# Kernel tuning notes

Measured on AMD Instinct MI355X. Metric: run time of the kernel, lower is better.

Reference implementation:

```python
import jax, jax.numpy as jnp
import numpy as np

EMBED_DIM = 1024
NUM_HEADS = 16
HEAD_DIM = EMBED_DIM // NUM_HEADS


def setup_inputs() -> dict:
    key = jax.random.key(0)
    ks = jax.random.split(key, 9)
    B, S, E = 4, 2048, EMBED_DIM
    # xavier_uniform bound for square [E, E] weights
    bound = float(np.sqrt(6.0 / (E + E)))
    def w(k):
        return jax.random.uniform(k, (E, E), jnp.float32, -bound, bound)
    return {
        "x": jax.random.normal(ks[0], (B, S, E), jnp.float32),
        "Wq": w(ks[1]), "bq": jnp.zeros((E,), jnp.float32),
        "Wk": w(ks[2]), "bk": jnp.zeros((E,), jnp.float32),
        "Wv": w(ks[3]), "bv": jnp.zeros((E,), jnp.float32),
        "Wo": w(ks[4]), "bo": jnp.zeros((E,), jnp.float32),
    }


def reference(x, Wq, bq, Wk, bk, Wv, bv, Wo, bo):
    B, S, E = x.shape
    H, D = NUM_HEADS, HEAD_DIM
    # Linear projections (torch Linear: x @ W.T + b)
    q = (x @ Wq.T + bq).reshape(B, S, H, D)
    k = (x @ Wk.T + bk).reshape(B, S, H, D)
    v = (x @ Wv.T + bv).reshape(B, S, H, D)
    # per-head scaled dot-product attention (vectorized over heads)
    scores = jnp.einsum("bqhd,bkhd->bhqk", q, k) / jnp.sqrt(jnp.float32(D))
    attn = jax.nn.softmax(scores, axis=-1)
    o = jnp.einsum("bhqk,bkhd->bqhd", attn, v).reshape(B, S, E)
    return o @ Wo.T + bo
```

## Files before the change

kernel.cpp:

```cpp
#include <hip/hip_runtime.h>
#include <stdint.h>

typedef unsigned short u16;
typedef short bf16x8 __attribute__((ext_vector_type(8)));
typedef float f32x4 __attribute__((ext_vector_type(4)));

#define B_ 4
#define S_ 2048
#define H_ 16
#define D_ 64
#define E_ 1024
#define M_ (B_ * S_)

static __device__ __forceinline__ u16 f2bf(float f) {
  uint32_t u = __builtin_bit_cast(uint32_t, f);
  u += 0x7fffu + ((u >> 16) & 1u);
  return (u16)(u >> 16);
}
static __device__ __forceinline__ u16 hu16(float f) {
  return (u16)((__builtin_bit_cast(uint32_t, f) + 0x8000u) >> 16);
}
static __device__ __forceinline__ uint32_t pack2bf(float a, float b) {
  return (uint32_t)f2bf(a) | ((uint32_t)f2bf(b) << 16);
}

static __device__ __forceinline__ void gld_lds16(const void* g, void* l) {
  __builtin_amdgcn_global_load_lds(
      (const __attribute__((address_space(1))) void*)(uintptr_t)g,
      (__attribute__((address_space(3))) void*)(uint32_t)(uintptr_t)l, 16, 0, 0);
}

template <int ctrl>
static __device__ __forceinline__ float dpp_mov(float x) {
  return __builtin_bit_cast(float,
      __builtin_amdgcn_update_dpp(0, __builtin_bit_cast(int, x), ctrl, 0xF, 0xF, true));
}
static __device__ __forceinline__ float rowsum16(float x) {
  x += dpp_mov<0xB1>(x);
  x += dpp_mov<0x4E>(x);
  x += dpp_mov<0x141>(x);
  x += dpp_mov<0x140>(x);
  return x;
}

#define NXE (M_ * E_)
#define NWE (E_ * E_)
__global__ __launch_bounds__(256) void cvt_all(const float* __restrict__ x,
                                               const float* __restrict__ Wq,
                                               const float* __restrict__ Wk,
                                               const float* __restrict__ Wv,
                                               const float* __restrict__ Wo,
                                               u16* __restrict__ ws) {
  int i = (blockIdx.x * 256 + threadIdx.x) * 8;
  const float* src;
  u16* dst = ws + i;
  if (i < NXE) { src = x + i; }
  else if (i < NXE + NWE)     { src = Wq + (i - NXE); }
  else if (i < NXE + 2 * NWE) { src = Wk + (i - NXE - NWE); }
  else if (i < NXE + 3 * NWE) { src = Wv + (i - NXE - 2 * NWE); }
  else                        { src = Wo + (i - NXE - 3 * NWE); }
  float4 a = *(const float4*)src;
  float4 b = *(const float4*)(src + 4);
  struct __align__(16) U8 { u16 h[8]; } u;
  u.h[0] = f2bf(a.x); u.h[1] = f2bf(a.y); u.h[2] = f2bf(a.z); u.h[3] = f2bf(a.w);
  u.h[4] = f2bf(b.x); u.h[5] = f2bf(b.y); u.h[6] = f2bf(b.z); u.h[7] = f2bf(b.w);
  *(U8*)dst = u;
}

template <int KIND, typename OutT>
static __device__ __forceinline__ void gemm128(const u16* __restrict__ A,
                                               const u16* __restrict__ W,
                                               const float* __restrict__ bias,
                                               OutT* __restrict__ C, int m0, int n0,
                                               float scale, u16* As, u16* Bs) {
  const int tid = threadIdx.x;
  const int wave = tid >> 6, lane = tid & 63;
  const int col16 = lane & 15, quad = lane >> 4;
  const int wm = wave >> 1, wn = wave & 1;

  f32x4 acc[4][4] = {};

  const int r0 = tid >> 3;
  const int sg8 = ((tid & 7) ^ (r0 & 7)) * 8;
  const u16* ga = A + (size_t)(m0 + r0) * E_ + sg8;
  const u16* gb = W + (size_t)(n0 + r0) * E_ + sg8;
  u16* lA = As + wave * 512;
  u16* lB = Bs + wave * 512;

  for (int k0 = 0; k0 < E_; k0 += 64) {
    __syncthreads();
#pragma unroll
    for (int i = 0; i < 4; i++) {
      gld_lds16(ga + (size_t)(i * 32) * E_ + k0, lA + i * 2048);
      gld_lds16(gb + (size_t)(i * 32) * E_ + k0, lB + i * 2048);
    }
    asm volatile("s_waitcnt vmcnt(0)" ::: "memory");
    __syncthreads();

    bf16x8 af[4][2], bw[4][2];
#pragma unroll
    for (int mt = 0; mt < 4; mt++)
#pragma unroll
      for (int ks = 0; ks < 2; ks++)
        af[mt][ks] = *(const bf16x8*)&As[(wm * 64 + mt * 16 + col16) * 64 +
                                         (((ks * 4 + quad) ^ (col16 & 7)) * 8)];
#pragma unroll
    for (int nt = 0; nt < 4; nt++)
#pragma unroll
      for (int ks = 0; ks < 2; ks++)
        bw[nt][ks] = *(const bf16x8*)&Bs[(wn * 64 + nt * 16 + col16) * 64 +
                                         (((ks * 4 + quad) ^ (col16 & 7)) * 8)];
#pragma unroll
    for (int ks = 0; ks < 2; ks++)
#pragma unroll
      for (int a = 0; a < 4; a++)
#pragma unroll
        for (int b = 0; b < 4; b++) {
          if constexpr (KIND == 2)
            acc[a][b] = __builtin_amdgcn_mfma_f32_16x16x32_bf16(af[a][ks], bw[b][ks], acc[a][b], 0, 0, 0);
          else
            acc[a][b] = __builtin_amdgcn_mfma_f32_16x16x32_bf16(bw[a][ks], af[b][ks], acc[a][b], 0, 0, 0);
        }
  }

  if constexpr (KIND == 2) {
#pragma unroll
    for (int a = 0; a < 4; a++) {
      int t = m0 + wm * 64 + a * 16 + quad * 4;
      int bb = t >> 11, s = t & (S_ - 1);
#pragma unroll
      for (int b = 0; b < 4; b++) {
        int oc = n0 + wn * 64 + b * 16 + col16;
        int h = oc >> 6, d = oc & 63;
        float bv = bias[oc];
        uint2 pk = {pack2bf(acc[a][b][0] + bv, acc[a][b][1] + bv),
                    pack2bf(acc[a][b][2] + bv, acc[a][b][3] + bv)};
        *(uint2*)&C[(((size_t)(bb * H_ + h) * D_ + d) * S_) + s] = pk;
      }
    }
  } else {
#pragma unroll
    for (int b = 0; b < 4; b++) {
      int row = m0 + wm * 64 + b * 16 + col16;
#pragma unroll
      for (int a = 0; a < 4; a++) {
        int nc = n0 + wn * 64 + a * 16 + quad * 4;
        float4 bv = *(const float4*)&bias[nc];
        float v0 = (acc[a][b][0] + bv.x) * scale;
        float v1 = (acc[a][b][1] + bv.y) * scale;
        float v2 = (acc[a][b][2] + bv.z) * scale;
        float v3 = (acc[a][b][3] + bv.w) * scale;
        if constexpr (KIND == 0) {
          uint2 pk = {pack2bf(v0, v1), pack2bf(v2, v3)};
          *(uint2*)&((u16*)C)[(size_t)row * E_ + nc] = pk;
        } else {
          float4 pk = {v0, v1, v2, v3};
          *(float4*)&((float*)C)[(size_t)row * E_ + nc] = pk;
        }
      }
    }
  }
}

__global__ __launch_bounds__(256) void gemm_qkv(const u16* __restrict__ xb,
                                                const u16* __restrict__ wq, const u16* __restrict__ wk,
                                                const u16* __restrict__ wv,
                                                const float* __restrict__ bq, const float* __restrict__ bk,
                                                const float* __restrict__ bv,
                                                u16* __restrict__ Qb, u16* __restrict__ Kb,
                                                u16* __restrict__ Vtb) {
  __shared__ __align__(16) u16 As[128 * 64];
  __shared__ __align__(16) u16 Bs[128 * 64];
  const int mat = blockIdx.x >> 3;
  const int n0 = (blockIdx.x & 7) * 128;
  const int m0 = blockIdx.y * 128;
  if (mat == 0)
    gemm128<0, u16>(xb, wq, bq, Qb, m0, n0, 0.125f * 1.44269504f, As, Bs);
  else if (mat == 1)
    gemm128<0, u16>(xb, wk, bk, Kb, m0, n0, 1.0f, As, Bs);
  else
    gemm128<2, u16>(xb, wv, bv, Vtb, m0, n0, 1.0f, As, Bs);
}

__global__ __launch_bounds__(256) void gemm_out(const u16* __restrict__ Ob,
                                                const u16* __restrict__ wob,
                                                const float* __restrict__ bo,
                                                float* __restrict__ out) {
  __shared__ __align__(16) u16 As[128 * 64];
  __shared__ __align__(16) u16 Bs[128 * 64];
  gemm128<1, float>(Ob, wob, bo, out, blockIdx.y * 128, blockIdx.x * 128, 1.0f, As, Bs);
}

__global__ __launch_bounds__(256) void flash_attn(const u16* __restrict__ Q,
                                                  const u16* __restrict__ K,
                                                  const u16* __restrict__ Vt,
                                                  u16* __restrict__ O) {
  __shared__ __align__(16) u16 Ks[2][64 * 64];
  __shared__ __align__(16) u16 Vs[64 * 64];
  __shared__ __align__(16) u16 Ps[4][32 * 72];
  const int bid = blockIdx.x;
  const int qt = bid >> 6, h = bid & 15, b = (bid >> 4) & 3;
  const int tid = threadIdx.x;
  const int wave = tid >> 6, lane = tid & 63;
  const int col16 = lane & 15, quad = lane >> 4;

  bf16x8 qf[2][2];
  const int qrow = qt * 128 + wave * 32;
#pragma unroll
  for (int mt = 0; mt < 2; mt++) {
    const u16* qp = Q + ((size_t)(b * S_ + qrow + mt * 16 + col16) * H_ + h) * D_ + quad * 8;
    qf[mt][0] = *(const bf16x8*)qp;
    qf[mt][1] = *(const bf16x8*)(qp + 32);
  }

  f32x4 o_acc[2][4] = {};
  float l_i[2][4] = {};

  const int srow = tid >> 3;
  const int sgrp = (tid & 7) ^ (srow & 7);
  const u16* Kbase = K + ((size_t)(b * S_) * H_ + h) * D_;
  const u16* Vbase = Vt + ((size_t)(b * H_ + h) * D_) * S_;
  u16* Pw = &Ps[wave][0];

  auto stageK = [&](int kb, int buf) {
#pragma unroll
    for (int i = 0; i < 2; i++)
      gld_lds16(Kbase + (size_t)(kb * 64 + i * 32 + srow) * (H_ * D_) + sgrp * 8,
                &Ks[buf][i * 2048 + wave * 512]);
  };
  auto stageV = [&](int kb) {
#pragma unroll
    for (int i = 0; i < 2; i++)
      gld_lds16(Vbase + (size_t)(i * 32 + srow) * S_ + kb * 64 + sgrp * 8,
                &Vs[i * 2048 + wave * 512]);
  };

  stageK(0, 0);
  for (int kb = 0; kb < S_ / 64; kb++) {
    const int cur = kb & 1;
    asm volatile("s_barrier" ::: "memory");
    stageV(kb);
    stageK((kb + 1) & 31, cur ^ 1);
    asm volatile("s_waitcnt vmcnt(4)" ::: "memory");
    asm volatile("s_barrier" ::: "memory");
    const u16* KsC = Ks[cur];

    f32x4 sacc[2][4] = {};
#pragma unroll
    for (int ks = 0; ks < 2; ks++) {
      bf16x8 kf[4];
#pragma unroll
      for (int nt = 0; nt < 4; nt++)
        kf[nt] = *(const bf16x8*)&KsC[(nt * 16 + col16) * 64 +
                                      (((ks * 4 + quad) ^ (col16 & 7)) * 8)];
#pragma unroll
      for (int mt = 0; mt < 2; mt++)
#pragma unroll
        for (int nt = 0; nt < 4; nt++)
          sacc[mt][nt] = __builtin_amdgcn_mfma_f32_16x16x32_bf16(qf[mt][ks], kf[nt], sacc[mt][nt], 0, 0, 0);
    }

#pragma unroll
    for (int mt = 0; mt < 2; mt++) {
#pragma unroll
      for (int e = 0; e < 4; e++) {
        float p0 = __builtin_amdgcn_exp2f(sacc[mt][0][e]);
        float p1 = __builtin_amdgcn_exp2f(sacc[mt][1][e]);
        float p2 = __builtin_amdgcn_exp2f(sacc[mt][2][e]);
        float p3 = __builtin_amdgcn_exp2f(sacc[mt][3][e]);
        l_i[mt][e] += (p0 + p1) + (p2 + p3);
        const int r = mt * 16 + quad * 4 + e;
        const int ro = r * 72;
        const int cb = col16 + ((r & 8) ? 16 : 0);
        Pw[ro + (cb & 63)] = hu16(p0);
        Pw[ro + ((cb + 16) & 63)] = hu16(p1);
        Pw[ro + ((cb + 32) & 63)] = hu16(p2);
        Pw[ro + ((cb + 48) & 63)] = hu16(p3);
      }
    }
    asm volatile("s_waitcnt lgkmcnt(0)" ::: "memory");
    asm volatile("s_waitcnt vmcnt(2)" ::: "memory");
    asm volatile("s_barrier" ::: "memory");

#pragma unroll
    for (int ks = 0; ks < 2; ks++) {
      bf16x8 pf[2], vf[4];
#pragma unroll
      for (int mt = 0; mt < 2; mt++)
        pf[mt] = *(const bf16x8*)&Pw[(mt * 16 + col16) * 72 +
                                     (((ks * 4 + quad + ((col16 >> 3) << 1)) & 7) * 8)];
#pragma unroll
      for (int nt = 0; nt < 4; nt++)
        vf[nt] = *(const bf16x8*)&Vs[(nt * 16 + col16) * 64 +
                                     (((ks * 4 + quad) ^ (col16 & 7)) * 8)];
#pragma unroll
      for (int mt = 0; mt < 2; mt++)
#pragma unroll
        for (int nt = 0; nt < 4; nt++)
          o_acc[mt][nt] = __builtin_amdgcn_mfma_f32_16x16x32_bf16(pf[mt], vf[nt], o_acc[mt][nt], 0, 0, 0);
    }
  }

#pragma unroll
  for (int mt = 0; mt < 2; mt++) {
#pragma unroll
    for (int e = 0; e < 4; e++) {
      float inv = 1.f / rowsum16(l_i[mt][e]);
      int s = qrow + mt * 16 + quad * 4 + e;
#pragma unroll
      for (int nt = 0; nt < 4; nt++)
        O[((size_t)(b * S_ + s) * H_ + h) * D_ + nt * 16 + col16] =
            f2bf(o_acc[mt][nt][e] * inv);
    }
  }
}

extern "C" void kernel_launch(void* const* d_in, const int* in_sizes, int n_in,
                              void* d_out, int out_size, void* d_ws, size_t ws_size,
                              hipStream_t stream) {
  (void)in_sizes; (void)n_in; (void)out_size; (void)ws_size;
  const float* x  = (const float*)d_in[0];
  const float* Wq = (const float*)d_in[1];
  const float* bq = (const float*)d_in[2];
  const float* Wk = (const float*)d_in[3];
  const float* bk = (const float*)d_in[4];
  const float* Wv = (const float*)d_in[5];
  const float* bv = (const float*)d_in[6];
  const float* Wo = (const float*)d_in[7];
  const float* bo = (const float*)d_in[8];
  float* out = (float*)d_out;

  const size_t NX = (size_t)M_ * E_;
  const size_t NW = (size_t)E_ * E_;
  u16* xb  = (u16*)d_ws;
  u16* wqb = xb + NX;
  u16* wkb = wqb + NW;
  u16* wvb = wkb + NW;
  u16* wob = wvb + NW;
  u16* Qb  = wob + NW;
  u16* Kb  = Qb + NX;
  u16* Vtb = Kb + NX;
  u16* Ob  = Vtb + NX;

  cvt_all<<<(NX + 4 * NW) / 2048, 256, 0, stream>>>(x, Wq, Wk, Wv, Wo, xb);

  gemm_qkv<<<dim3(24, 64), 256, 0, stream>>>(xb, wqb, wkb, wvb, bq, bk, bv, Qb, Kb, Vtb);
  flash_attn<<<B_ * H_ * (S_ / 128), 256, 0, stream>>>(Qb, Kb, Vtb, Ob);
  gemm_out<<<dim3(8, 64), 256, 0, stream>>>(Ob, wob, bo, out);
}
```

Measured before the change: 307.1 us.

## Compute transposed scores with 32x32x8 MFMA and keep P in registers

Flash attention now uses 32x32x8 bf16 MFMAs computing S^T = K·Q^T, so each lane's score outputs line up with the B-operand layout needed for the P·V MFMA. P is packed to bf16 in registers and fed straight into the second matmul, which removes the per-wave LDS staging buffer for P, its stores and reloads, and the lgkmcnt wait. The row-sum reduction becomes a single cross-half shuffle and O is written with vectorized stores. The tradeoff is that 32x32x8 MFMAs use smaller K-steps, so more MFMA instructions and LDS reads are issued, and register pressure rises with f32x16 accumulators.

```diff
diff --git a/kernel.cpp b/kernel.cpp
--- a/kernel.cpp
+++ b/kernel.cpp
@@ -2,8 +2,10 @@
 #include <stdint.h>
 
 typedef unsigned short u16;
+typedef short bf16x4 __attribute__((ext_vector_type(4)));
 typedef short bf16x8 __attribute__((ext_vector_type(8)));
 typedef float f32x4 __attribute__((ext_vector_type(4)));
+typedef float f32x16 __attribute__((ext_vector_type(16)));
 
 #define B_ 4
 #define S_ 2048
@@ -17,11 +19,13 @@
   u += 0x7fffu + ((u >> 16) & 1u);
   return (u16)(u >> 16);
 }
-static __device__ __forceinline__ u16 hu16(float f) {
-  return (u16)((__builtin_bit_cast(uint32_t, f) + 0x8000u) >> 16);
-}
 static __device__ __forceinline__ uint32_t pack2bf(float a, float b) {
   return (uint32_t)f2bf(a) | ((uint32_t)f2bf(b) << 16);
+}
+static __device__ __forceinline__ uint32_t pk_hu(float a, float b) {
+  uint32_t ua = __builtin_bit_cast(uint32_t, a) + 0x8000u;
+  uint32_t ub = __builtin_bit_cast(uint32_t, b) + 0x8000u;
+  return __builtin_amdgcn_perm(ub, ua, 0x07060302u);
 }
 
 static __device__ __forceinline__ void gld_lds16(const void* g, void* l) {
@@ -30,17 +34,13 @@
       (__attribute__((address_space(3))) void*)(uint32_t)(uintptr_t)l, 16, 0, 0);
 }
 
-template <int ctrl>
-static __device__ __forceinline__ float dpp_mov(float x) {
-  return __builtin_bit_cast(float,
-      __builtin_amdgcn_update_dpp(0, __builtin_bit_cast(int, x), ctrl, 0xF, 0xF, true));
-}
-static __device__ __forceinline__ float rowsum16(float x) {
-  x += dpp_mov<0xB1>(x);
-  x += dpp_mov<0x4E>(x);
-  x += dpp_mov<0x141>(x);
-  x += dpp_mov<0x140>(x);
-  return x;
+static __device__ __forceinline__ f32x16 mfma32x8(bf16x4 a, bf16x4 b, f32x16 c) {
+#if __has_builtin(__builtin_amdgcn_mfma_f32_32x32x8bf16_1k)
+  return __builtin_amdgcn_mfma_f32_32x32x8bf16_1k(a, b, c, 0, 0, 0);
+#else
+  asm volatile("v_mfma_f32_32x32x8_bf16 %0, %1, %2, %0" : "+v"(c) : "v"(a), "v"(b));
+  return c;
+#endif
 }
 
 #define NXE (M_ * E_)
@@ -197,30 +197,25 @@
                                                   u16* __restrict__ O) {
   __shared__ __align__(16) u16 Ks[2][64 * 64];
   __shared__ __align__(16) u16 Vs[64 * 64];
-  __shared__ __align__(16) u16 Ps[4][32 * 72];
   const int bid = blockIdx.x;
   const int qt = bid >> 6, h = bid & 15, b = (bid >> 4) & 3;
   const int tid = threadIdx.x;
   const int wave = tid >> 6, lane = tid & 63;
-  const int col16 = lane & 15, quad = lane >> 4;
-
-  bf16x8 qf[2][2];
-  const int qrow = qt * 128 + wave * 32;
-#pragma unroll
-  for (int mt = 0; mt < 2; mt++) {
-    const u16* qp = Q + ((size_t)(b * S_ + qrow + mt * 16 + col16) * H_ + h) * D_ + quad * 8;
-    qf[mt][0] = *(const bf16x8*)qp;
-    qf[mt][1] = *(const bf16x8*)(qp + 32);
-  }
-
-  f32x4 o_acc[2][4] = {};
-  float l_i[2][4] = {};
+  const int ln = lane & 31, half = lane >> 5;
+  const int q = qt * 128 + wave * 32 + ln;
+
+  bf16x4 qf[8];
+  const u16* qp = Q + ((size_t)(b * S_ + q) * H_ + h) * D_ + half * 4;
+#pragma unroll
+  for (int s = 0; s < 8; s++) qf[s] = *(const bf16x4*)(qp + 8 * s);
+
+  f32x16 oT[2] = {};
+  float l = 0.f;
 
   const int srow = tid >> 3;
   const int sgrp = (tid & 7) ^ (srow & 7);
   const u16* Kbase = K + ((size_t)(b * S_) * H_ + h) * D_;
   const u16* Vbase = Vt + ((size_t)(b * H_ + h) * D_) * S_;
-  u16* Pw = &Ps[wave][0];
 
   auto stageK = [&](int kb, int buf) {
 #pragma unroll
@@ -236,6 +231,8 @@
   };
 
   stageK(0, 0);
+  asm volatile("s_waitcnt vmcnt(2)" ::: "memory");
+
   for (int kb = 0; kb < S_ / 64; kb++) {
     const int cur = kb & 1;
     asm volatile("s_barrier" ::: "memory");
@@ -243,76 +240,53 @@
     stageK((kb + 1) & 31, cur ^ 1);
     asm volatile("s_waitcnt vmcnt(4)" ::: "memory");
     asm volatile("s_barrier" ::: "memory");
-    const u16* KsC = Ks[cur];
-
-    f32x4 sacc[2][4] = {};
-#pragma unroll
-    for (int ks = 0; ks < 2; ks++) {
-      bf16x8 kf[4];
-#pragma unroll
-      for (int nt = 0; nt < 4; nt++)
-        kf[nt] = *(const bf16x8*)&KsC[(nt * 16 + col16) * 64 +
-                                      (((ks * 4 + quad) ^ (col16 & 7)) * 8)];
-#pragma unroll
-      for (int mt = 0; mt < 2; mt++)
-#pragma unroll
-        for (int nt = 0; nt < 4; nt++)
-          sacc[mt][nt] = __builtin_amdgcn_mfma_f32_16x16x32_bf16(qf[mt][ks], kf[nt], sacc[mt][nt], 0, 0, 0);
-    }
-
-#pragma unroll
-    for (int mt = 0; mt < 2; mt++) {
-#pragma unroll
-      for (int e = 0; e < 4; e++) {
-        float p0 = __builtin_amdgcn_exp2f(sacc[mt][0][e]);
-        float p1 = __builtin_amdgcn_exp2f(sacc[mt][1][e]);
-        float p2 = __builtin_amdgcn_exp2f(sacc[mt][2][e]);
-        float p3 = __builtin_amdgcn_exp2f(sacc[mt][3][e]);
-        l_i[mt][e] += (p0 + p1) + (p2 + p3);
-        const int r = mt * 16 + quad * 4 + e;
-        const int ro = r * 72;
-        const int cb = col16 + ((r & 8) ? 16 : 0);
-        Pw[ro + (cb & 63)] = hu16(p0);
-        Pw[ro + ((cb + 16) & 63)] = hu16(p1);
-        Pw[ro + ((cb + 32) & 63)] = hu16(p2);
-        Pw[ro + ((cb + 48) & 63)] = hu16(p3);
-      }
-    }
-    asm volatile("s_waitcnt lgkmcnt(0)" ::: "memory");
+
+    bf16x4 pt[2][4];
+#pragma unroll
+    for (int kt = 0; kt < 2; kt++) {
+      f32x16 st = {};
+#pragma unroll
+      for (int s = 0; s < 8; s++) {
+        bf16x4 kf = *(const bf16x4*)&Ks[cur][(kt * 32 + ln) * 64 +
+                                             ((s ^ (ln & 7)) * 8 + half * 4)];
+        st = mfma32x8(kf, qf[s], st);
+      }
+#pragma unroll
+      for (int g = 0; g < 4; g++) {
+        float p0 = __builtin_amdgcn_exp2f(st[4 * g + 0]);
+        float p1 = __builtin_amdgcn_exp2f(st[4 * g + 1]);
+        float p2 = __builtin_amdgcn_exp2f(st[4 * g + 2]);
+        float p3 = __builtin_amdgcn_exp2f(st[4 * g + 3]);
+        l += (p0 + p1) + (p2 + p3);
+        uint32_t lo = pk_hu(p0, p1), hi = pk_hu(p2, p3);
+        pt[kt][g] = __builtin_bit_cast(bf16x4, make_uint2(lo, hi));
+      }
+    }
+
     asm volatile("s_waitcnt vmcnt(2)" ::: "memory");
     asm volatile("s_barrier" ::: "memory");
 
 #pragma unroll
-    for (int ks = 0; ks < 2; ks++) {
-      bf16x8 pf[2], vf[4];
-#pragma unroll
-      for (int mt = 0; mt < 2; mt++)
-        pf[mt] = *(const bf16x8*)&Pw[(mt * 16 + col16) * 72 +
-                                     (((ks * 4 + quad + ((col16 >> 3) << 1)) & 7) * 8)];
-#pragma unroll
-      for (int nt = 0; nt < 4; nt++)
-        vf[nt] = *(const bf16x8*)&Vs[(nt * 16 + col16) * 64 +
-                                     (((ks * 4 + quad) ^ (col16 & 7)) * 8)];
-#pragma unroll
-      for (int mt = 0; mt < 2; mt++)
-#pragma unroll
-        for (int nt = 0; nt < 4; nt++)
-          o_acc[mt][nt] = __builtin_amdgcn_mfma_f32_16x16x32_bf16(pf[mt], vf[nt], o_acc[mt][nt], 0, 0, 0);
-    }
+    for (int dt = 0; dt < 2; dt++)
+#pragma unroll
+      for (int sp = 0; sp < 8; sp++) {
+        bf16x4 vf = *(const bf16x4*)&Vs[(dt * 32 + ln) * 64 +
+                                        ((sp ^ (ln & 7)) * 8 + half * 4)];
+        oT[dt] = mfma32x8(vf, pt[sp >> 2][sp & 3], oT[dt]);
+      }
   }
 
-#pragma unroll
-  for (int mt = 0; mt < 2; mt++) {
-#pragma unroll
-    for (int e = 0; e < 4; e++) {
-      float inv = 1.f / rowsum16(l_i[mt][e]);
-      int s = qrow + mt * 16 + quad * 4 + e;
-#pragma unroll
-      for (int nt = 0; nt < 4; nt++)
-        O[((size_t)(b * S_ + s) * H_ + h) * D_ + nt * 16 + col16] =
-            f2bf(o_acc[mt][nt][e] * inv);
-    }
-  }
+  float inv = 1.f / (l + __shfl_xor(l, 32));
+  u16* Obase = O + ((size_t)(b * S_ + q) * H_ + h) * D_;
+#pragma unroll
+  for (int dt = 0; dt < 2; dt++)
+#pragma unroll
+    for (int g = 0; g < 4; g++) {
+      int d = dt * 32 + 8 * g + half * 4;
+      uint2 pk = {pack2bf(oT[dt][4 * g + 0] * inv, oT[dt][4 * g + 1] * inv),
+                  pack2bf(oT[dt][4 * g + 2] * inv, oT[dt][4 * g + 3] * inv)};
+      *(uint2*)(Obase + d) = pk;
+    }
 }
 
 extern "C" void kernel_launch(void* const* d_in, const int* in_sizes, int n_in,
```

Result: slower. 316.0 us (+2.9%).

## Double-buffer GEMM K-tiles and double attention query rows per wave

Applied to the files above, without the earlier changes.

The shared GEMM routine now uses a K-step of 32 with two LDS buffers, so the next tile loads while MFMAs run on the current one. This replaces the old load, wait-all, compute sequence. Flash attention now gives each wave 64 query rows instead of 32, reusing every staged K/V tile across twice the queries and halving the grid. The cost is more registers, a larger P buffer in LDS, fewer blocks in flight, and twice as many barriers in the GEMM K loop.

```diff
diff --git a/kernel.cpp b/kernel.cpp
--- a/kernel.cpp
+++ b/kernel.cpp
@@ -80,47 +80,49 @@
 
   f32x4 acc[4][4] = {};
 
-  const int r0 = tid >> 3;
-  const int sg8 = ((tid & 7) ^ (r0 & 7)) * 8;
+  const int r0 = tid >> 2;
+  const int sg8 = ((tid & 3) ^ (r0 & 3)) * 8;
   const u16* ga = A + (size_t)(m0 + r0) * E_ + sg8;
   const u16* gb = W + (size_t)(n0 + r0) * E_ + sg8;
-  u16* lA = As + wave * 512;
-  u16* lB = Bs + wave * 512;
-
-  for (int k0 = 0; k0 < E_; k0 += 64) {
-    __syncthreads();
-#pragma unroll
-    for (int i = 0; i < 4; i++) {
-      gld_lds16(ga + (size_t)(i * 32) * E_ + k0, lA + i * 2048);
-      gld_lds16(gb + (size_t)(i * 32) * E_ + k0, lB + i * 2048);
-    }
-    asm volatile("s_waitcnt vmcnt(0)" ::: "memory");
-    __syncthreads();
-
-    bf16x8 af[4][2], bw[4][2];
+
+  auto stage = [&](int it, int buf) {
+    u16* dA = As + buf * 4096 + wave * 512;
+    u16* dB = Bs + buf * 4096 + wave * 512;
+    const int k0 = it * 32;
+    gld_lds16(ga + k0, dA);
+    gld_lds16(ga + k0 + (size_t)64 * E_, dA + 2048);
+    gld_lds16(gb + k0, dB);
+    gld_lds16(gb + k0 + (size_t)64 * E_, dB + 2048);
+  };
+
+  stage(0, 0);
+  for (int it = 0; it < 32; it++) {
+    const int cur = it & 1;
+    stage(it + 1 < 32 ? it + 1 : 31, cur ^ 1);
+    asm volatile("s_waitcnt vmcnt(4)" ::: "memory");
+    asm volatile("s_barrier" ::: "memory");
+    const u16* LA = As + cur * 4096;
+    const u16* LB = Bs + cur * 4096;
+
+    bf16x8 af[4], bw[4];
 #pragma unroll
     for (int mt = 0; mt < 4; mt++)
-#pragma unroll
-      for (int ks = 0; ks < 2; ks++)
-        af[mt][ks] = *(const bf16x8*)&As[(wm * 64 + mt * 16 + col16) * 64 +
-                                         (((ks * 4 + quad) ^ (col16 & 7)) * 8)];
+      af[mt] = *(const bf16x8*)&LA[(wm * 64 + mt * 16 + col16) * 32 +
+                                   ((quad ^ (col16 & 3)) * 8)];
 #pragma unroll
     for (int nt = 0; nt < 4; nt++)
-#pragma unroll
-      for (int ks = 0; ks < 2; ks++)
-        bw[nt][ks] = *(const bf16x8*)&Bs[(wn * 64 + nt * 16 + col16) * 64 +
-                                         (((ks * 4 + quad) ^ (col16 & 7)) * 8)];
-#pragma unroll
-    for (int ks = 0; ks < 2; ks++)
-#pragma unroll
-      for (int a = 0; a < 4; a++)
-#pragma unroll
-        for (int b = 0; b < 4; b++) {
-          if constexpr (KIND == 2)
-            acc[a][b] = __builtin_amdgcn_mfma_f32_16x16x32_bf16(af[a][ks], bw[b][ks], acc[a][b], 0, 0, 0);
-          else
-            acc[a][b] = __builtin_amdgcn_mfma_f32_16x16x32_bf16(bw[a][ks], af[b][ks], acc[a][b], 0, 0, 0);
-        }
+      bw[nt] = *(const bf16x8*)&LB[(wn * 64 + nt * 16 + col16) * 32 +
+                                   ((quad ^ (col16 & 3)) * 8)];
+#pragma unroll
+    for (int a = 0; a < 4; a++)
+#pragma unroll
+      for (int b = 0; b < 4; b++) {
+        if constexpr (KIND == 2)
+          acc[a][b] = __builtin_amdgcn_mfma_f32_16x16x32_bf16(af[a], bw[b], acc[a][b], 0, 0, 0);
+        else
+          acc[a][b] = __builtin_amdgcn_mfma_f32_16x16x32_bf16(bw[a], af[b], acc[a][b], 0, 0, 0);
+      }
+    asm volatile("s_barrier" ::: "memory");
   }
 
   if constexpr (KIND == 2) {
@@ -169,8 +171,8 @@
                                                 const float* __restrict__ bv,
                                                 u16* __restrict__ Qb, u16* __restrict__ Kb,
                                                 u16* __restrict__ Vtb) {
-  __shared__ __align__(16) u16 As[128 * 64];
-  __shared__ __align__(16) u16 Bs[128 * 64];
+  __shared__ __align__(16) u16 As[2 * 128 * 32];
+  __shared__ __align__(16) u16 Bs[2 * 128 * 32];
   const int mat = blockIdx.x >> 3;
   const int n0 = (blockIdx.x & 7) * 128;
   const int m0 = blockIdx.y * 128;
@@ -186,8 +188,8 @@
                                                 const u16* __restrict__ wob,
                                                 const float* __restrict__ bo,
                                                 float* __restrict__ out) {
-  __shared__ __align__(16) u16 As[128 * 64];
-  __shared__ __align__(16) u16 Bs[128 * 64];
+  __shared__ __align__(16) u16 As[2 * 128 * 32];
+  __shared__ __align__(16) u16 Bs[2 * 128 * 32];
   gemm128<1, float>(Ob, wob, bo, out, blockIdx.y * 128, blockIdx.x * 128, 1.0f, As, Bs);
 }
 
@@ -197,24 +199,24 @@
                                                   u16* __restrict__ O) {
   __shared__ __align__(16) u16 Ks[2][64 * 64];
   __shared__ __align__(16) u16 Vs[64 * 64];
-  __shared__ __align__(16) u16 Ps[4][32 * 72];
+  __shared__ __align__(16) u16 Ps[4][64 * 72];
   const int bid = blockIdx.x;
   const int qt = bid >> 6, h = bid & 15, b = (bid >> 4) & 3;
   const int tid = threadIdx.x;
   const int wave = tid >> 6, lane = tid & 63;
   const int col16 = lane & 15, quad = lane >> 4;
 
-  bf16x8 qf[2][2];
-  const int qrow = qt * 128 + wave * 32;
-#pragma unroll
-  for (int mt = 0; mt < 2; mt++) {
+  bf16x8 qf[4][2];
+  const int qrow = qt * 256 + wave * 64;
+#pragma unroll
+  for (int mt = 0; mt < 4; mt++) {
     const u16* qp = Q + ((size_t)(b * S_ + qrow + mt * 16 + col16) * H_ + h) * D_ + quad * 8;
     qf[mt][0] = *(const bf16x8*)qp;
     qf[mt][1] = *(const bf16x8*)(qp + 32);
   }
 
-  f32x4 o_acc[2][4] = {};
-  float l_i[2][4] = {};
+  f32x4 o_acc[4][4] = {};
+  float l_i[4][4] = {};
 
   const int srow = tid >> 3;
   const int sgrp = (tid & 7) ^ (srow & 7);
@@ -245,29 +247,28 @@
     asm volatile("s_barrier" ::: "memory");
     const u16* KsC = Ks[cur];
 
-    f32x4 sacc[2][4] = {};
-#pragma unroll
-    for (int ks = 0; ks < 2; ks++) {
-      bf16x8 kf[4];
+    bf16x8 kf[2][4];
+#pragma unroll
+    for (int ks = 0; ks < 2; ks++)
 #pragma unroll
       for (int nt = 0; nt < 4; nt++)
-        kf[nt] = *(const bf16x8*)&KsC[(nt * 16 + col16) * 64 +
-                                      (((ks * 4 + quad) ^ (col16 & 7)) * 8)];
-#pragma unroll
-      for (int mt = 0; mt < 2; mt++)
+        kf[ks][nt] = *(const bf16x8*)&KsC[(nt * 16 + col16) * 64 +
+                                          (((ks * 4 + quad) ^ (col16 & 7)) * 8)];
+
+#pragma unroll
+    for (int mt = 0; mt < 4; mt++) {
+      f32x4 sacc[4] = {};
+#pragma unroll
+      for (int ks = 0; ks < 2; ks++)
 #pragma unroll
         for (int nt = 0; nt < 4; nt++)
-          sacc[mt][nt] = __builtin_amdgcn_mfma_f32_16x16x32_bf16(qf[mt][ks], kf[nt], sacc[mt][nt], 0, 0, 0);
-    }
-
-#pragma unroll
-    for (int mt = 0; mt < 2; mt++) {
+          sacc[nt] = __builtin_amdgcn_mfma_f32_16x16x32_bf16(qf[mt][ks], kf[ks][nt], sacc[nt], 0, 0, 0);
 #pragma unroll
       for (int e = 0; e < 4; e++) {
-        float p0 = __builtin_amdgcn_exp2f(sacc[mt][0][e]);
-        float p1 = __builtin_amdgcn_exp2f(sacc[mt][1][e]);
-        float p2 = __builtin_amdgcn_exp2f(sacc[mt][2][e]);
-        float p3 = __builtin_amdgcn_exp2f(sacc[mt][3][e]);
+        float p0 = __builtin_amdgcn_exp2f(sacc[0][e]);
+        float p1 = __builtin_amdgcn_exp2f(sacc[1][e]);
+        float p2 = __builtin_amdgcn_exp2f(sacc[2][e]);
+        float p3 = __builtin_amdgcn_exp2f(sacc[3][e]);
         l_i[mt][e] += (p0 + p1) + (p2 + p3);
         const int r = mt * 16 + quad * 4 + e;
         const int ro = r * 72;
@@ -282,27 +283,30 @@
     asm volatile("s_waitcnt vmcnt(2)" ::: "memory");
     asm volatile("s_barrier" ::: "memory");
 
-#pragma unroll
-    for (int ks = 0; ks < 2; ks++) {
-      bf16x8 pf[2], vf[4];
-#pragma unroll
-      for (int mt = 0; mt < 2; mt++)
-        pf[mt] = *(const bf16x8*)&Pw[(mt * 16 + col16) * 72 +
+    bf16x8 vf[2][4];
+#pragma unroll
+    for (int ks = 0; ks < 2; ks++)
+#pragma unroll
+      for (int nt = 0; nt < 4; nt++)
+        vf[ks][nt] = *(const bf16x8*)&Vs[(nt * 16 + col16) * 64 +
+                                         (((ks * 4 + quad) ^ (col16 & 7)) * 8)];
+#pragma unroll
+    for (int mt = 0; mt < 4; mt++) {
+      bf16x8 pf[2];
+#pragma unroll
+      for (int ks = 0; ks < 2; ks++)
+        pf[ks] = *(const bf16x8*)&Pw[(mt * 16 + col16) * 72 +
                                      (((ks * 4 + quad + ((col16 >> 3) << 1)) & 7) * 8)];
 #pragma unroll
-      for (int nt = 0; nt < 4; nt++)
-        vf[nt] = *(const bf16x8*)&Vs[(nt * 16 + col16) * 64 +
-                                     (((ks * 4 + quad) ^ (col16 & 7)) * 8)];
-#pragma unroll
-      for (int mt = 0; mt < 2; mt++)
+      for (int ks = 0; ks < 2; ks++)
 #pragma unroll
         for (int nt = 0; nt < 4; nt++)
-          o_acc[mt][nt] = __builtin_amdgcn_mfma_f32_16x16x32_bf16(pf[mt], vf[nt], o_acc[mt][nt], 0, 0, 0);
-    }
-  }
-
-#pragma unroll
-  for (int mt = 0; mt < 2; mt++) {
+          o_acc[mt][nt] = __builtin_amdgcn_mfma_f32_16x16x32_bf16(pf[ks], vf[ks][nt], o_acc[mt][nt], 0, 0, 0);
+    }
+  }
+
+#pragma unroll
+  for (int mt = 0; mt < 4; mt++) {
 #pragma unroll
     for (int e = 0; e < 4; e++) {
       float inv = 1.f / rowsum16(l_i[mt][e]);
@@ -345,6 +349,6 @@
   cvt_all<<<(NX + 4 * NW) / 2048, 256, 0, stream>>>(x, Wq, Wk, Wv, Wo, xb);
 
   gemm_qkv<<<dim3(24, 64), 256, 0, stream>>>(xb, wqb, wkb, wvb, bq, bk, bv, Qb, Kb, Vtb);
-  flash_attn<<<B_ * H_ * (S_ / 128), 256, 0, stream>>>(Qb, Kb, Vtb, Ob);
+  flash_attn<<<4 * 16 * (S_ / 256), 256, 0, stream>>>(Qb, Kb, Vtb, Ob);
   gemm_out<<<dim3(8, 64), 256, 0, stream>>>(Ob, wob, bo, out);
 }
```

Result: slower. 344.2 us (+12.1%).
